# Kernel tuning notes

Measured on AMD Instinct MI355X. Metric: run time of the kernel, lower is better.

## Reference

```python
import jax, jax.numpy as jnp
import numpy as np

VOCAB = 32000
EMB = 512
HID = 512
MAX_LEN = 32
SOS = 1
PAD = 0


def setup_inputs() -> dict:
    key = jax.random.key(0)
    ks = jax.random.split(key, 9)
    s = 1.0 / np.sqrt(HID)
    emb = jax.random.normal(ks[0], (VOCAB, EMB), jnp.float32)
    emb = emb.at[PAD].set(0.0)  # padding_idx row is zeros
    return {
        "encoder_hidden": jax.random.normal(ks[1], (1, 64, HID), jnp.float32),
        "encoder_c": jax.random.normal(ks[2], (1, 64, HID), jnp.float32),
        "emb": emb,
        "W_ih": jax.random.uniform(ks[3], (4 * HID, EMB), jnp.float32, -s, s),
        "W_hh": jax.random.uniform(ks[4], (4 * HID, HID), jnp.float32, -s, s),
        "b_ih": jax.random.uniform(ks[5], (4 * HID,), jnp.float32, -s, s),
        "b_hh": jax.random.uniform(ks[6], (4 * HID,), jnp.float32, -s, s),
        "fc_w": jax.random.uniform(ks[7], (VOCAB, HID), jnp.float32, -s, s),
        "fc_b": jax.random.uniform(ks[8], (VOCAB,), jnp.float32, -s, s),
    }


def reference(encoder_hidden, encoder_c, emb, W_ih, W_hh, b_ih, b_hh, fc_w, fc_b):
    B = encoder_hidden.shape[1]
    h0 = encoder_hidden[0]  # [B,H] (num_layers == 1)
    c0 = encoder_c[0]
    tok0 = jnp.full((B,), SOS, jnp.int32)
    bias = b_ih + b_hh  # [4H]

    def step(carry, _):
        tok, h, c = carry
        x = emb[tok]  # [B,E] embedding gather
        gates = x @ W_ih.T + h @ W_hh.T + bias  # [B,4H]
        i, f, g, o = jnp.split(gates, 4, axis=-1)  # torch gate order i,f,g,o
        c = jax.nn.sigmoid(f) * c + jax.nn.sigmoid(i) * jnp.tanh(g)
        h = jax.nn.sigmoid(o) * jnp.tanh(c)
        logp = jax.nn.log_softmax(h @ fc_w.T + fc_b, axis=-1)  # [B,V]
        tok_next = jnp.argmax(logp, axis=-1).astype(jnp.int32)  # greedy topk(k=1)
        return (tok_next, h, c), logp

    (_, hT, _), logps = jax.lax.scan(step, (tok0, h0, c0), None, length=MAX_LEN + 1)
    decoder_outputs = jnp.transpose(logps, (1, 0, 2))  # [B, T, V]
    decoder_hidden = hT[None]  # [1, B, H]
    return decoder_outputs, decoder_hidden
```

## Files before the change

kernel.cpp:

```cpp
#include <hip/hip_runtime.h>
#include <math.h>

#define VOCABN 32000
#define HIDN 512
#define BN 64
#define TSTEPS 33
#define OUTROWS (TSTEPS * VOCABN)
#define NVBLK 500
#define NVT 2000

typedef float f4 __attribute__((ext_vector_type(4)));
typedef __bf16 bf16x8 __attribute__((ext_vector_type(8)));
typedef unsigned short u16x8 __attribute__((ext_vector_type(8)));

__device__ __forceinline__ unsigned short f2bf_rn(float f) {
    unsigned int u = __builtin_bit_cast(unsigned int, f);
    u += 0x7FFFu + ((u >> 16) & 1u);
    return (unsigned short)(u >> 16);
}
__device__ __forceinline__ float bfbits2f(unsigned short s) {
    unsigned int u = ((unsigned int)s) << 16;
    return __builtin_bit_cast(float, u);
}

__global__ __launch_bounds__(256) void k_init(const float* __restrict__ eh,
                                              const float* __restrict__ ec,
                                              float* __restrict__ h,
                                              float* __restrict__ c,
                                              int* __restrict__ tok) {
    int i = blockIdx.x * 256 + threadIdx.x;
    if (i < BN * HIDN) { h[i] = eh[i]; c[i] = ec[i]; }
    if (i < BN) tok[i] = 1;
}

__global__ __launch_bounds__(256) void k_conv(const float* __restrict__ fc_w,
                                              unsigned short* __restrict__ whiP,
                                              unsigned short* __restrict__ wloP) {
    const int vt = blockIdx.x;
    const int tid = threadIdx.x;
    #pragma unroll
    for (int i = 0; i < 4; ++i) {
        const int s = tid + 256 * i;
        const int kc = s >> 6, lane = s & 63;
        const int v = vt * 16 + (lane & 15);
        const int k = kc * 32 + (lane >> 4) * 8;
        const float* src = fc_w + (size_t)v * 512 + k;
        f4 a = *(const f4*)src;
        f4 b = *(const f4*)(src + 4);
        u16x8 hi, lo;
        #pragma unroll
        for (int e = 0; e < 4; ++e) {
            unsigned short ha = f2bf_rn(a[e]);
            hi[e] = ha; lo[e] = f2bf_rn(a[e] - bfbits2f(ha));
            unsigned short hb = f2bf_rn(b[e]);
            hi[4 + e] = hb; lo[4 + e] = f2bf_rn(b[e] - bfbits2f(hb));
        }
        const size_t o = ((size_t)(vt * 16 + kc) * 64 + lane) * 8;
        *(u16x8*)&whiP[o] = hi;
        *(u16x8*)&wloP[o] = lo;
    }
}

__global__ __launch_bounds__(256) void k_gates(const float* __restrict__ W_ih,
                                               const float* __restrict__ W_hh,
                                               const float* __restrict__ emb,
                                               const float* __restrict__ h,
                                               const int* __restrict__ tok,
                                               float* __restrict__ part) {
    __shared__ float w_s[64][68];
    __shared__ float x_s[64][68];
    const int tid = threadIdx.x;
    const int j0 = (blockIdx.x & 31) * 64;
    const int ks = blockIdx.x >> 5;
    const int k0 = ks * 256;
    const int tx = tid & 15;
    const int ty = tid >> 4;
    const int r  = tid >> 2;
    const int cq = (tid & 3) * 16;

    float acc[4][4];
    #pragma unroll
    for (int i = 0; i < 4; ++i)
        #pragma unroll
        for (int j = 0; j < 4; ++j) acc[i][j] = 0.f;

    for (int kk = 0; kk < 256; kk += 64) {
        const int k = k0 + kk;
        __syncthreads();
        {
            const float* src = (k < 512) ? (W_ih + (size_t)(j0 + r) * 512 + k + cq)
                                         : (W_hh + (size_t)(j0 + r) * 512 + (k - 512) + cq);
            const f4* s4 = (const f4*)src;
            f4* d4 = (f4*)&w_s[r][cq];
            d4[0] = s4[0]; d4[1] = s4[1]; d4[2] = s4[2]; d4[3] = s4[3];
        }
        {
            const float* src = (k < 512) ? (emb + (size_t)tok[r] * 512 + k + cq)
                                         : (h + (size_t)r * 512 + (k - 512) + cq);
            const f4* s4 = (const f4*)src;
            f4* d4 = (f4*)&x_s[r][cq];
            d4[0] = s4[0]; d4[1] = s4[1]; d4[2] = s4[2]; d4[3] = s4[3];
        }
        __syncthreads();
        #pragma unroll 4
        for (int c4 = 0; c4 < 64; c4 += 4) {
            f4 wv[4], xv[4];
            #pragma unroll
            for (int jj = 0; jj < 4; ++jj) wv[jj] = *(const f4*)&w_s[16 * jj + tx][c4];
            #pragma unroll
            for (int bb = 0; bb < 4; ++bb) xv[bb] = *(const f4*)&x_s[16 * bb + ty][c4];
            #pragma unroll
            for (int e = 0; e < 4; ++e)
                #pragma unroll
                for (int bb = 0; bb < 4; ++bb)
                    #pragma unroll
                    for (int jj = 0; jj < 4; ++jj)
                        acc[bb][jj] += xv[bb][e] * wv[jj][e];
        }
    }
    #pragma unroll
    for (int bb = 0; bb < 4; ++bb) {
        const int b = 16 * bb + ty;
        #pragma unroll
        for (int jj = 0; jj < 4; ++jj)
            part[((size_t)(ks * 64 + b)) * 2048 + j0 + 16 * jj + tx] = acc[bb][jj];
    }
}

__device__ __forceinline__ float sigf(float x) { return 1.f / (1.f + expf(-x)); }

__global__ __launch_bounds__(256) void k_cell(const float* __restrict__ part,
                                              const float* __restrict__ b_ih,
                                              const float* __restrict__ b_hh,
                                              float* __restrict__ h,
                                              float* __restrict__ c,
                                              unsigned short* __restrict__ hhi,
                                              unsigned short* __restrict__ hlo) {
    const int e = blockIdx.x * 256 + threadIdx.x;
    const int b = e >> 9, u = e & 511;
    float g[4];
    #pragma unroll
    for (int gi = 0; gi < 4; ++gi) {
        const int j = gi * 512 + u;
        float s = b_ih[j] + b_hh[j];
        #pragma unroll
        for (int ks = 0; ks < 4; ++ks) s += part[((size_t)(ks * 64 + b)) * 2048 + j];
        g[gi] = s;
    }
    const float ig = sigf(g[0]);
    const float fg = sigf(g[1]);
    const float gg = tanhf(g[2]);
    const float og = sigf(g[3]);
    const float cn = fg * c[e] + ig * gg;
    const float hn = og * tanhf(cn);
    c[e] = cn;
    h[e] = hn;
    const unsigned short hi = f2bf_rn(hn);
    hhi[e] = hi;
    hlo[e] = f2bf_rn(hn - bfbits2f(hi));
}

__device__ __forceinline__ void olmerge(float& m, float& s, int& idx,
                                        float mo, float so, int io) {
    float M = fmaxf(m, mo);
    s = s * __expf(m - M) + so * __expf(mo - M);
    idx = (mo > m) ? io : ((mo == m) ? (io < idx ? io : idx) : idx);
    m = M;
}

__global__ __launch_bounds__(256) void k_logits(const unsigned short* __restrict__ whiP,
                                                const unsigned short* __restrict__ wloP,
                                                const float* __restrict__ fc_b,
                                                const unsigned short* __restrict__ hhi,
                                                const unsigned short* __restrict__ hlo,
                                                float* __restrict__ outrow,
                                                float* __restrict__ pm,
                                                float* __restrict__ ps,
                                                int* __restrict__ pi) {
    __shared__ float red_m[4 * 64];
    __shared__ float red_s[4 * 64];
    __shared__ int   red_i[4 * 64];

    const int tid  = threadIdx.x;
    const int w    = tid >> 6;
    const int lane = tid & 63;
    const int li   = lane & 15;
    const int lg   = lane >> 4;
    const int vt   = blockIdx.x * 4 + w;

    f4 acc[4];
    #pragma unroll
    for (int bf = 0; bf < 4; ++bf) acc[bf] = (f4){0.f, 0.f, 0.f, 0.f};

    const unsigned short* Ah = whiP + (size_t)vt * 8192 + lane * 8;
    const unsigned short* Al = wloP + (size_t)vt * 8192 + lane * 8;
    int boff[4];
    #pragma unroll
    for (int bf = 0; bf < 4; ++bf) boff[bf] = (li + 16 * bf) * 512 + lg * 8;

    #pragma unroll 4
    for (int kc = 0; kc < 16; ++kc) {
        bf16x8 Avh = *(const bf16x8*)(Ah + kc * 512);
        bf16x8 Avl = *(const bf16x8*)(Al + kc * 512);
        #pragma unroll
        for (int bf = 0; bf < 4; ++bf) {
            bf16x8 Bh = *(const bf16x8*)&hhi[boff[bf] + kc * 32];
            bf16x8 Bl = *(const bf16x8*)&hlo[boff[bf] + kc * 32];
            acc[bf] = __builtin_amdgcn_mfma_f32_16x16x32_bf16(Avh, Bh, acc[bf], 0, 0, 0);
            acc[bf] = __builtin_amdgcn_mfma_f32_16x16x32_bf16(Avl, Bh, acc[bf], 0, 0, 0);
            acc[bf] = __builtin_amdgcn_mfma_f32_16x16x32_bf16(Avh, Bl, acc[bf], 0, 0, 0);
        }
    }

    const int vbase = vt * 16;
    const f4 bias = *(const f4*)&fc_b[vbase + lg * 4];

    #pragma unroll
    for (int bf = 0; bf < 4; ++bf) {
        f4 x = acc[bf] + bias;
        acc[bf] = x;
        const int b = li + 16 * bf;
        *(f4*)&outrow[(size_t)b * OUTROWS + vbase + lg * 4] = x;
    }

    #pragma unroll
    for (int bf = 0; bf < 4; ++bf) {
        float m = -1e30f; int idx = 0;
        #pragma unroll
        for (int rg = 0; rg < 4; ++rg) {
            float x = acc[bf][rg];
            if (x > m) { m = x; idx = vbase + lg * 4 + rg; }
        }
        float s = 0.f;
        #pragma unroll
        for (int rg = 0; rg < 4; ++rg) s += __expf(acc[bf][rg] - m);
        #pragma unroll
        for (int off = 16; off <= 32; off <<= 1) {
            float mo = __shfl_xor(m, off);
            float so = __shfl_xor(s, off);
            int   io = __shfl_xor(idx, off);
            olmerge(m, s, idx, mo, so, io);
        }
        if (lg == 0) {
            red_m[w * 64 + li + 16 * bf] = m;
            red_s[w * 64 + li + 16 * bf] = s;
            red_i[w * 64 + li + 16 * bf] = idx;
        }
    }
    __syncthreads();
    if (tid < 64) {
        float m = red_m[tid]; float s = red_s[tid]; int idx = red_i[tid];
        #pragma unroll
        for (int w2 = 1; w2 < 4; ++w2)
            olmerge(m, s, idx, red_m[w2 * 64 + tid], red_s[w2 * 64 + tid], red_i[w2 * 64 + tid]);
        pm[blockIdx.x * 64 + tid] = m;
        ps[blockIdx.x * 64 + tid] = s;
        pi[blockIdx.x * 64 + tid] = idx;
    }
}

__global__ __launch_bounds__(256) void k_combine(const float* __restrict__ pm,
                                                 const float* __restrict__ ps,
                                                 const int* __restrict__ pi,
                                                 int* __restrict__ tok,
                                                 float* __restrict__ Lb, int t) {
    __shared__ float sm[256], ss[256];
    __shared__ int si[256];
    const int b = blockIdx.x;
    const int tid = threadIdx.x;
    float m = -1e30f, s = 0.f; int idx = 0;
    for (int blk = tid; blk < NVBLK; blk += 256)
        olmerge(m, s, idx, pm[blk * 64 + b], ps[blk * 64 + b], pi[blk * 64 + b]);
    sm[tid] = m; ss[tid] = s; si[tid] = idx;
    __syncthreads();
    for (int st = 128; st; st >>= 1) {
        if (tid < st) {
            float m0 = sm[tid], s0 = ss[tid]; int i0 = si[tid];
            olmerge(m0, s0, i0, sm[tid + st], ss[tid + st], si[tid + st]);
            sm[tid] = m0; ss[tid] = s0; si[tid] = i0;
        }
        __syncthreads();
    }
    if (tid == 0) { tok[b] = si[0]; Lb[t * 64 + b] = sm[0] + logf(ss[0]); }
}

__global__ __launch_bounds__(256) void k_sub(float* __restrict__ out,
                                             const float* __restrict__ Lb) {
    const int N4 = BN * OUTROWS / 4;
    for (int i4 = blockIdx.x * 256 + threadIdx.x; i4 < N4; i4 += gridDim.x * 256) {
        const int i = i4 * 4;
        const int b = i / OUTROWS;
        const int rem = i - b * OUTROWS;
        const int t = rem / VOCABN;
        f4 x = *(const f4*)&out[i];
        const float L = Lb[t * 64 + b];
        x[0] -= L; x[1] -= L; x[2] -= L; x[3] -= L;
        *(f4*)&out[i] = x;
    }
}

__global__ __launch_bounds__(256) void k_copyh(const float* __restrict__ h,
                                               float* __restrict__ dst) {
    int i = blockIdx.x * 256 + threadIdx.x;
    if (i < BN * HIDN) dst[i] = h[i];
}

__global__ __launch_bounds__(256) void k_logits_f32(const float* __restrict__ fc_w,
                                                    const float* __restrict__ fc_b,
                                                    const float* __restrict__ h,
                                                    float* __restrict__ outrow) {
    __shared__ float w_s[64][68];
    __shared__ float h_s[64][68];
    const int tid = threadIdx.x;
    const int v0 = blockIdx.x * 64;
    const int tx = tid & 15;
    const int ty = tid >> 4;
    const int r  = tid >> 2;
    const int cq = (tid & 3) * 16;

    float acc[4][4];
    #pragma unroll
    for (int i = 0; i < 4; ++i)
        #pragma unroll
        for (int j = 0; j < 4; ++j) acc[i][j] = 0.f;

    for (int k = 0; k < 512; k += 64) {
        __syncthreads();
        {
            const f4* s4 = (const f4*)(fc_w + (size_t)(v0 + r) * 512 + k + cq);
            f4* d4 = (f4*)&w_s[r][cq];
            d4[0] = s4[0]; d4[1] = s4[1]; d4[2] = s4[2]; d4[3] = s4[3];
        }
        {
            const f4* s4 = (const f4*)(h + (size_t)r * 512 + k + cq);
            f4* d4 = (f4*)&h_s[r][cq];
            d4[0] = s4[0]; d4[1] = s4[1]; d4[2] = s4[2]; d4[3] = s4[3];
        }
        __syncthreads();
        #pragma unroll 4
        for (int c4 = 0; c4 < 64; c4 += 4) {
            f4 wv[4], hv[4];
            #pragma unroll
            for (int vv = 0; vv < 4; ++vv) wv[vv] = *(const f4*)&w_s[16 * vv + tx][c4];
            #pragma unroll
            for (int bb = 0; bb < 4; ++bb) hv[bb] = *(const f4*)&h_s[16 * bb + ty][c4];
            #pragma unroll
            for (int e = 0; e < 4; ++e)
                #pragma unroll
                for (int bb = 0; bb < 4; ++bb)
                    #pragma unroll
                    for (int vv = 0; vv < 4; ++vv)
                        acc[bb][vv] += hv[bb][e] * wv[vv][e];
        }
    }
    float bias[4];
    #pragma unroll
    for (int vv = 0; vv < 4; ++vv) bias[vv] = fc_b[v0 + 16 * vv + tx];
    #pragma unroll
    for (int bb = 0; bb < 4; ++bb) {
        const int b = 16 * bb + ty;
        #pragma unroll
        for (int vv = 0; vv < 4; ++vv)
            outrow[(size_t)b * OUTROWS + v0 + 16 * vv + tx] = acc[bb][vv] + bias[vv];
    }
}

__global__ __launch_bounds__(1024) void k_softmax(float* __restrict__ outrow,
                                                  int* __restrict__ tok) {
    const int b = blockIdx.x, tid = threadIdx.x;
    float* row = outrow + (size_t)b * OUTROWS;
    __shared__ float sm[1024];
    __shared__ int si[1024];

    float m = -1e30f; int mi = 0;
    for (int v = tid; v < VOCABN; v += 1024) {
        float x = row[v];
        if (x > m) { m = x; mi = v; }
    }
    sm[tid] = m; si[tid] = mi;
    __syncthreads();
    for (int s = 512; s; s >>= 1) {
        if (tid < s) {
            float xo = sm[tid + s]; int io = si[tid + s];
            if (xo > sm[tid] || (xo == sm[tid] && io < si[tid])) { sm[tid] = xo; si[tid] = io; }
        }
        __syncthreads();
    }
    const float M = sm[0];
    const int ami = si[0];
    __syncthreads();

    float sum = 0.f;
    for (int v = tid; v < VOCABN; v += 1024) sum += __expf(row[v] - M);
    sm[tid] = sum;
    __syncthreads();
    for (int s = 512; s; s >>= 1) {
        if (tid < s) sm[tid] += sm[tid + s];
        __syncthreads();
    }
    const float L = M + logf(sm[0]);
    if (tid == 0) tok[b] = ami;

    for (int v = tid; v < VOCABN; v += 1024) row[v] = row[v] - L;
}

extern "C" void kernel_launch(void* const* d_in, const int* in_sizes, int n_in,
                              void* d_out, int out_size, void* d_ws, size_t ws_size,
                              hipStream_t stream) {
    const float* enc_h = (const float*)d_in[0];
    const float* enc_c = (const float*)d_in[1];
    const float* emb   = (const float*)d_in[2];
    const float* W_ih  = (const float*)d_in[3];
    const float* W_hh  = (const float*)d_in[4];
    const float* b_ih  = (const float*)d_in[5];
    const float* b_hh  = (const float*)d_in[6];
    const float* fc_w  = (const float*)d_in[7];
    const float* fc_b  = (const float*)d_in[8];
    float* out = (float*)d_out;

    float* ws   = (float*)d_ws;
    float* h    = ws;
    float* c    = h + 32768;
    float* part = c + 32768;
    unsigned short* hhi = (unsigned short*)(part + 524288);
    unsigned short* hlo = hhi + 32768;
    float* pm   = (float*)(hlo + 32768);
    float* ps   = pm + 32000;
    int*   pi   = (int*)(ps + 32000);
    float* Lb   = (float*)(pi + 32000);
    int*   tok  = (int*)(Lb + 2112);
    unsigned short* whiP = (unsigned short*)(tok + 64);
    unsigned short* wloP = whiP + (size_t)NVT * 8192;

    const size_t NEED = (size_t)((char*)(wloP + (size_t)NVT * 8192) - (char*)d_ws);

    if (ws_size >= NEED) {
        k_conv<<<NVT, 256, 0, stream>>>(fc_w, whiP, wloP);
        k_init<<<128, 256, 0, stream>>>(enc_h, enc_c, h, c, tok);
        for (int t = 0; t < TSTEPS; ++t) {
            k_gates<<<128, 256, 0, stream>>>(W_ih, W_hh, emb, h, tok, part);
            k_cell<<<128, 256, 0, stream>>>(part, b_ih, b_hh, h, c, hhi, hlo);
            float* outrow = out + (size_t)t * VOCABN;
            k_logits<<<NVBLK, 256, 0, stream>>>(whiP, wloP, fc_b, hhi, hlo, outrow, pm, ps, pi);
            k_combine<<<64, 256, 0, stream>>>(pm, ps, pi, tok, Lb, t);
        }
        k_sub<<<2048, 256, 0, stream>>>(out, Lb);
        k_copyh<<<128, 256, 0, stream>>>(h, out + (size_t)BN * OUTROWS);
    } else {
        k_init<<<128, 256, 0, stream>>>(enc_h, enc_c, h, c, tok);
        for (int t = 0; t < TSTEPS; ++t) {
            k_gates<<<128, 256, 0, stream>>>(W_ih, W_hh, emb, h, tok, part);
            k_cell<<<128, 256, 0, stream>>>(part, b_ih, b_hh, h, c, hhi, hlo);
            float* outrow = out + (size_t)t * VOCABN;
            k_logits_f32<<<500, 256, 0, stream>>>(fc_w, fc_b, h, outrow);
            k_softmax<<<64, 1024, 0, stream>>>(outrow, tok);
        }
        k_copyh<<<128, 256, 0, stream>>>(h, out + (size_t)BN * OUTROWS);
    }
}
```

Measured before the change: 2.173 ms.

## Fold argmax combine into gates kernel, defer logsumexp, stage logits via LDS

```diff
diff --git a/kernel.cpp b/kernel.cpp
--- a/kernel.cpp
+++ b/kernel.cpp
@@ -65,11 +65,34 @@
                                                const float* __restrict__ W_hh,
                                                const float* __restrict__ emb,
                                                const float* __restrict__ h,
-                                               const int* __restrict__ tok,
-                                               float* __restrict__ part) {
+                                               const float* __restrict__ pmT,
+                                               const int* __restrict__ piT,
+                                               float* __restrict__ part,
+                                               int t) {
     __shared__ float w_s[64][68];
     __shared__ float x_s[64][68];
+    __shared__ int tok_s[64];
     const int tid = threadIdx.x;
+
+    if (t > 0) {
+        const float* pmrow = pmT + (size_t)(t - 1) * (NVBLK * 64);
+        const int*   pirow = piT + (size_t)(t - 1) * (NVBLK * 64);
+        const int row = tid >> 2, q = tid & 3;
+        float m = -1e30f; int idx = 0;
+        for (int blk = q; blk < NVBLK; blk += 4) {
+            float mo = pmrow[blk * 64 + row];
+            int   io = pirow[blk * 64 + row];
+            if (mo > m || (mo == m && io < idx)) { m = mo; idx = io; }
+        }
+        #pragma unroll
+        for (int off = 1; off <= 2; off <<= 1) {
+            float mo = __shfl_xor(m, off);
+            int   io = __shfl_xor(idx, off);
+            if (mo > m || (mo == m && io < idx)) { m = mo; idx = io; }
+        }
+        if (q == 0) tok_s[row] = idx;
+    }
+
     const int j0 = (blockIdx.x & 31) * 64;
     const int ks = blockIdx.x >> 5;
     const int k0 = ks * 256;
@@ -95,7 +118,8 @@
             d4[0] = s4[0]; d4[1] = s4[1]; d4[2] = s4[2]; d4[3] = s4[3];
         }
         {
-            const float* src = (k < 512) ? (emb + (size_t)tok[r] * 512 + k + cq)
+            const int tk = (t > 0) ? tok_s[r] : 1;
+            const float* src = (k < 512) ? (emb + (size_t)tk * 512 + k + cq)
                                          : (h + (size_t)r * 512 + (k - 512) + cq);
             const f4* s4 = (const f4*)src;
             f4* d4 = (f4*)&x_s[r][cq];
@@ -174,12 +198,14 @@
                                                 const unsigned short* __restrict__ hhi,
                                                 const unsigned short* __restrict__ hlo,
                                                 float* __restrict__ outrow,
-                                                float* __restrict__ pm,
-                                                float* __restrict__ ps,
-                                                int* __restrict__ pi) {
-    __shared__ float red_m[4 * 64];
-    __shared__ float red_s[4 * 64];
-    __shared__ int   red_i[4 * 64];
+                                                float* __restrict__ pmT,
+                                                float* __restrict__ psT,
+                                                int* __restrict__ piT,
+                                                int t) {
+    __shared__ unsigned short smem[2][16384];
+    __shared__ float red_m[256];
+    __shared__ float red_s[256];
+    __shared__ int   red_i[256];
 
     const int tid  = threadIdx.x;
     const int w    = tid >> 6;
@@ -192,24 +218,43 @@
     #pragma unroll
     for (int bf = 0; bf < 4; ++bf) acc[bf] = (f4){0.f, 0.f, 0.f, 0.f};
 
-    const unsigned short* Ah = whiP + (size_t)vt * 8192 + lane * 8;
-    const unsigned short* Al = wloP + (size_t)vt * 8192 + lane * 8;
-    int boff[4];
-    #pragma unroll
-    for (int bf = 0; bf < 4; ++bf) boff[bf] = (li + 16 * bf) * 512 + lg * 8;
-
-    #pragma unroll 4
-    for (int kc = 0; kc < 16; ++kc) {
-        bf16x8 Avh = *(const bf16x8*)(Ah + kc * 512);
-        bf16x8 Avl = *(const bf16x8*)(Al + kc * 512);
-        #pragma unroll
-        for (int bf = 0; bf < 4; ++bf) {
-            bf16x8 Bh = *(const bf16x8*)&hhi[boff[bf] + kc * 32];
-            bf16x8 Bl = *(const bf16x8*)&hlo[boff[bf] + kc * 32];
-            acc[bf] = __builtin_amdgcn_mfma_f32_16x16x32_bf16(Avh, Bh, acc[bf], 0, 0, 0);
-            acc[bf] = __builtin_amdgcn_mfma_f32_16x16x32_bf16(Avl, Bh, acc[bf], 0, 0, 0);
-            acc[bf] = __builtin_amdgcn_mfma_f32_16x16x32_bf16(Avh, Bl, acc[bf], 0, 0, 0);
-        }
+    auto stage = [&](int ch, int buf) {
+        unsigned short* sb = smem[buf];
+        #pragma unroll
+        for (int kc = 0; kc < 2; ++kc) {
+            const size_t arow = ((size_t)(vt * 16 + ch * 2 + kc) * 64 + lane) * 8;
+            __builtin_amdgcn_global_load_lds(whiP + arow, &sb[(w * 4 + kc * 2 + 0) * 512], 16, 0, 0);
+            __builtin_amdgcn_global_load_lds(wloP + arow, &sb[(w * 4 + kc * 2 + 1) * 512], 16, 0, 0);
+        }
+        #pragma unroll
+        for (int j = 0; j < 4; ++j) {
+            const int f  = w * 4 + j;
+            const int kc = f >> 3, bf = (f >> 1) & 3, pl = f & 1;
+            const unsigned short* H = pl ? hlo : hhi;
+            const size_t boff = (size_t)(bf * 16 + li) * 512 + (ch * 2 + kc) * 32 + lg * 8;
+            __builtin_amdgcn_global_load_lds(H + boff, &sb[(16 + f) * 512], 16, 0, 0);
+        }
+    };
+
+    stage(0, 0);
+    __syncthreads();
+    for (int ch = 0; ch < 8; ++ch) {
+        if (ch < 7) stage(ch + 1, (ch + 1) & 1);
+        const unsigned short* sb = smem[ch & 1];
+        #pragma unroll
+        for (int kc = 0; kc < 2; ++kc) {
+            bf16x8 Ah = *(const bf16x8*)&sb[(w * 4 + kc * 2 + 0) * 512 + lane * 8];
+            bf16x8 Al = *(const bf16x8*)&sb[(w * 4 + kc * 2 + 1) * 512 + lane * 8];
+            #pragma unroll
+            for (int bf = 0; bf < 4; ++bf) {
+                bf16x8 Bh = *(const bf16x8*)&sb[(16 + kc * 8 + bf * 2 + 0) * 512 + lane * 8];
+                bf16x8 Bl = *(const bf16x8*)&sb[(16 + kc * 8 + bf * 2 + 1) * 512 + lane * 8];
+                acc[bf] = __builtin_amdgcn_mfma_f32_16x16x32_bf16(Ah, Bh, acc[bf], 0, 0, 0);
+                acc[bf] = __builtin_amdgcn_mfma_f32_16x16x32_bf16(Al, Bh, acc[bf], 0, 0, 0);
+                acc[bf] = __builtin_amdgcn_mfma_f32_16x16x32_bf16(Ah, Bl, acc[bf], 0, 0, 0);
+            }
+        }
+        __syncthreads();
     }
 
     const int vbase = vt * 16;
@@ -253,35 +298,40 @@
         #pragma unroll
         for (int w2 = 1; w2 < 4; ++w2)
             olmerge(m, s, idx, red_m[w2 * 64 + tid], red_s[w2 * 64 + tid], red_i[w2 * 64 + tid]);
-        pm[blockIdx.x * 64 + tid] = m;
-        ps[blockIdx.x * 64 + tid] = s;
-        pi[blockIdx.x * 64 + tid] = idx;
-    }
-}
-
-__global__ __launch_bounds__(256) void k_combine(const float* __restrict__ pm,
-                                                 const float* __restrict__ ps,
-                                                 const int* __restrict__ pi,
-                                                 int* __restrict__ tok,
-                                                 float* __restrict__ Lb, int t) {
+        const size_t o = (size_t)t * (NVBLK * 64) + blockIdx.x * 64 + tid;
+        pmT[o] = m;
+        psT[o] = s;
+        piT[o] = idx;
+    }
+}
+
+__global__ __launch_bounds__(256) void k_combineL(const float* __restrict__ pmT,
+                                                  const float* __restrict__ psT,
+                                                  float* __restrict__ Lb) {
     __shared__ float sm[256], ss[256];
-    __shared__ int si[256];
-    const int b = blockIdx.x;
+    const int t = blockIdx.x >> 6, b = blockIdx.x & 63;
     const int tid = threadIdx.x;
-    float m = -1e30f, s = 0.f; int idx = 0;
-    for (int blk = tid; blk < NVBLK; blk += 256)
-        olmerge(m, s, idx, pm[blk * 64 + b], ps[blk * 64 + b], pi[blk * 64 + b]);
-    sm[tid] = m; ss[tid] = s; si[tid] = idx;
+    const float* pmr = pmT + (size_t)t * (NVBLK * 64);
+    const float* psr = psT + (size_t)t * (NVBLK * 64);
+    float m = -1e30f, s = 0.f;
+    for (int blk = tid; blk < NVBLK; blk += 256) {
+        float mo = pmr[blk * 64 + b], so = psr[blk * 64 + b];
+        float M = fmaxf(m, mo);
+        s = s * __expf(m - M) + so * __expf(mo - M);
+        m = M;
+    }
+    sm[tid] = m; ss[tid] = s;
     __syncthreads();
     for (int st = 128; st; st >>= 1) {
         if (tid < st) {
-            float m0 = sm[tid], s0 = ss[tid]; int i0 = si[tid];
-            olmerge(m0, s0, i0, sm[tid + st], ss[tid + st], si[tid + st]);
-            sm[tid] = m0; ss[tid] = s0; si[tid] = i0;
-        }
-        __syncthreads();
-    }
-    if (tid == 0) { tok[b] = si[0]; Lb[t * 64 + b] = sm[0] + logf(ss[0]); }
+            float mo = sm[tid + st], so = ss[tid + st];
+            float M = fmaxf(sm[tid], mo);
+            ss[tid] = ss[tid] * __expf(sm[tid] - M) + so * __expf(mo - M);
+            sm[tid] = M;
+        }
+        __syncthreads();
+    }
+    if (tid == 0) Lb[t * 64 + b] = sm[0] + logf(ss[0]);
 }
 
 __global__ __launch_bounds__(256) void k_sub(float* __restrict__ out,
@@ -303,6 +353,72 @@
                                                float* __restrict__ dst) {
     int i = blockIdx.x * 256 + threadIdx.x;
     if (i < BN * HIDN) dst[i] = h[i];
+}
+
+__global__ __launch_bounds__(256) void k_gates_fb(const float* __restrict__ W_ih,
+                                                  const float* __restrict__ W_hh,
+                                                  const float* __restrict__ emb,
+                                                  const float* __restrict__ h,
+                                                  const int* __restrict__ tok,
+                                                  float* __restrict__ part) {
+    __shared__ float w_s[64][68];
+    __shared__ float x_s[64][68];
+    const int tid = threadIdx.x;
+    const int j0 = (blockIdx.x & 31) * 64;
+    const int ks = blockIdx.x >> 5;
+    const int k0 = ks * 256;
+    const int tx = tid & 15;
+    const int ty = tid >> 4;
+    const int r  = tid >> 2;
+    const int cq = (tid & 3) * 16;
+
+    float acc[4][4];
+    #pragma unroll
+    for (int i = 0; i < 4; ++i)
+        #pragma unroll
+        for (int j = 0; j < 4; ++j) acc[i][j] = 0.f;
+
+    for (int kk = 0; kk < 256; kk += 64) {
+        const int k = k0 + kk;
+        __syncthreads();
+        {
+            const float* src = (k < 512) ? (W_ih + (size_t)(j0 + r) * 512 + k + cq)
+                                         : (W_hh + (size_t)(j0 + r) * 512 + (k - 512) + cq);
+            const f4* s4 = (const f4*)src;
+            f4* d4 = (f4*)&w_s[r][cq];
+            d4[0] = s4[0]; d4[1] = s4[1]; d4[2] = s4[2]; d4[3] = s4[3];
+        }
+        {
+            const float* src = (k < 512) ? (emb + (size_t)tok[r] * 512 + k + cq)
+                                         : (h + (size_t)r * 512 + (k - 512) + cq);
+            const f4* s4 = (const f4*)src;
+            f4* d4 = (f4*)&x_s[r][cq];
+            d4[0] = s4[0]; d4[1] = s4[1]; d4[2] = s4[2]; d4[3] = s4[3];
+        }
+        __syncthreads();
+        #pragma unroll 4
+        for (int c4 = 0; c4 < 64; c4 += 4) {
+            f4 wv[4], xv[4];
+            #pragma unroll
+            for (int jj = 0; jj < 4; ++jj) wv[jj] = *(const f4*)&w_s[16 * jj + tx][c4];
+            #pragma unroll
+            for (int bb = 0; bb < 4; ++bb) xv[bb] = *(const f4*)&x_s[16 * bb + ty][c4];
+            #pragma unroll
+            for (int e = 0; e < 4; ++e)
+                #pragma unroll
+                for (int bb = 0; bb < 4; ++bb)
+                    #pragma unroll
+                    for (int jj = 0; jj < 4; ++jj)
+                        acc[bb][jj] += xv[bb][e] * wv[jj][e];
+        }
+    }
+    #pragma unroll
+    for (int bb = 0; bb < 4; ++bb) {
+        const int b = 16 * bb + ty;
+        #pragma unroll
+        for (int jj = 0; jj < 4; ++jj)
+            part[((size_t)(ks * 64 + b)) * 2048 + j0 + 16 * jj + tx] = acc[bb][jj];
+    }
 }
 
 __global__ __launch_bounds__(256) void k_logits_f32(const float* __restrict__ fc_w,
@@ -418,38 +534,38 @@
     const float* fc_b  = (const float*)d_in[8];
     float* out = (float*)d_out;
 
-    float* ws   = (float*)d_ws;
-    float* h    = ws;
-    float* c    = h + 32768;
-    float* part = c + 32768;
-    unsigned short* hhi = (unsigned short*)(part + 524288);
-    unsigned short* hlo = hhi + 32768;
-    float* pm   = (float*)(hlo + 32768);
-    float* ps   = pm + 32000;
-    int*   pi   = (int*)(ps + 32000);
-    float* Lb   = (float*)(pi + 32000);
-    int*   tok  = (int*)(Lb + 2112);
-    unsigned short* whiP = (unsigned short*)(tok + 64);
-    unsigned short* wloP = whiP + (size_t)NVT * 8192;
-
-    const size_t NEED = (size_t)((char*)(wloP + (size_t)NVT * 8192) - (char*)d_ws);
+    char* cur = (char*)d_ws;
+    float* h    = (float*)cur;            cur += 32768 * 4;
+    float* c    = (float*)cur;            cur += 32768 * 4;
+    float* part = (float*)cur;            cur += 524288 * 4;
+    unsigned short* hhi = (unsigned short*)cur; cur += 32768 * 2;
+    unsigned short* hlo = (unsigned short*)cur; cur += 32768 * 2;
+    float* pmT  = (float*)cur;            cur += (size_t)TSTEPS * NVBLK * 64 * 4;
+    float* psT  = (float*)cur;            cur += (size_t)TSTEPS * NVBLK * 64 * 4;
+    int*   piT  = (int*)cur;              cur += (size_t)TSTEPS * NVBLK * 64 * 4;
+    float* Lb   = (float*)cur;            cur += TSTEPS * 64 * 4;
+    int*   tok  = (int*)cur;              cur += 64 * 4;
+    unsigned short* whiP = (unsigned short*)cur; cur += (size_t)NVT * 8192 * 2;
+    unsigned short* wloP = (unsigned short*)cur; cur += (size_t)NVT * 8192 * 2;
+    const size_t NEED = (size_t)(cur - (char*)d_ws);
 
     if (ws_size >= NEED) {
         k_conv<<<NVT, 256, 0, stream>>>(fc_w, whiP, wloP);
         k_init<<<128, 256, 0, stream>>>(enc_h, enc_c, h, c, tok);
         for (int t = 0; t < TSTEPS; ++t) {
-            k_gates<<<128, 256, 0, stream>>>(W_ih, W_hh, emb, h, tok, part);
+            k_gates<<<128, 256, 0, stream>>>(W_ih, W_hh, emb, h, pmT, piT, part, t);
             k_cell<<<128, 256, 0, stream>>>(part, b_ih, b_hh, h, c, hhi, hlo);
             float* outrow = out + (size_t)t * VOCABN;
-            k_logits<<<NVBLK, 256, 0, stream>>>(whiP, wloP, fc_b, hhi, hlo, outrow, pm, ps, pi);
-            k_combine<<<64, 256, 0, stream>>>(pm, ps, pi, tok, Lb, t);
-        }
+            k_logits<<<NVBLK, 256, 0, stream>>>(whiP, wloP, fc_b, hhi, hlo, outrow,
+                                                pmT, psT, piT, t);
+        }
+        k_combineL<<<TSTEPS * 64, 256, 0, stream>>>(pmT, psT, Lb);
         k_sub<<<2048, 256, 0, stream>>>(out, Lb);
         k_copyh<<<128, 256, 0, stream>>>(h, out + (size_t)BN * OUTROWS);
     } else {
         k_init<<<128, 256, 0, stream>>>(enc_h, enc_c, h, c, tok);
         for (int t = 0; t < TSTEPS; ++t) {
-            k_gates<<<128, 256, 0, stream>>>(W_ih, W_hh, emb, h, tok, part);
+            k_gates_fb<<<128, 256, 0, stream>>>(W_ih, W_hh, emb, h, tok, part);
             k_cell<<<128, 256, 0, stream>>>(part, b_ih, b_hh, h, c, hhi, hlo);
             float* outrow = out + (size_t)t * VOCABN;
             k_logits_f32<<<500, 256, 0, stream>>>(fc_w, fc_b, h, outrow);
```

New measurement: 2.786 ms. 1.28x slower.
